# Performance work log

Measured on AMD Instinct MI355X. Metric: run time of the kernel, lower is better.

Reference implementation:

```python
import jax, jax.numpy as jnp
import numpy as np

B, LI, LC = 2, 1024, 256
H, NH, HD = 1024, 16, 64
MLP = 4096
EPS = 1e-6


def rmsnorm(x, w):
    return x * jax.lax.rsqrt(jnp.mean(x * x, axis=-1, keepdims=True) + EPS) * w


def apply_rope(x, cos, sin):
    # x: [B, NH, S, HD]; cos/sin: [S, HD]; rotate-half convention
    x1, x2 = jnp.split(x, 2, axis=-1)
    rot = jnp.concatenate([-x2, x1], axis=-1)
    return x * cos + rot * sin


def project_qkv(x, w, b):
    # x: [B, S, H] -> q,k,v each [B, NH, S, HD]
    bsz, s, _ = x.shape
    qkv = (x @ w.T + b).reshape(bsz, s, 3, NH, HD)
    qkv = jnp.transpose(qkv, (2, 0, 3, 1, 4))
    return qkv[0], qkv[1], qkv[2]


def setup_inputs() -> dict:
    key = jax.random.key(0)
    ks = iter(jax.random.split(key, 40))
    n = lambda shape, scale=1.0: jax.random.normal(next(ks), shape, dtype=jnp.float32) * scale
    xav = lambda fo, fi: n((fo, fi), float(np.sqrt(2.0 / (fo + fi))))
    inp = {
        'image_tokens': n((B, LI, H)),
        'condition_tokens': n((B, LC, H)),
        'image_rope_cos': n((LI, HD)),
        'image_rope_sin': n((LI, HD)),
        'cond_rope_cos': n((LC, HD)),
        'cond_rope_sin': n((LC, HD)),
        'img_norm1_w': jnp.ones((H,)), 'cond_norm1_w': jnp.ones((H,)),
        'img_qkv_w': xav(3 * H, H), 'img_qkv_b': jnp.zeros((3 * H,)),
        'cond_qkv_w': xav(3 * H, H), 'cond_qkv_b': jnp.zeros((3 * H,)),
        'img_qn_w': jnp.ones((HD,)), 'img_kn_w': jnp.ones((HD,)),
        'cond_qn_w': jnp.ones((HD,)), 'cond_kn_w': jnp.ones((HD,)),
        'img_out_w': xav(H, H), 'img_out_b': jnp.zeros((H,)),
        'cond_out_w': xav(H, H), 'cond_out_b': jnp.zeros((H,)),
        'img_norm2_w': jnp.ones((H,)), 'cond_norm2_w': jnp.ones((H,)),
        'img_mlp_w1': xav(MLP, H), 'img_mlp_b1': jnp.zeros((MLP,)),
        'img_mlp_w2': xav(MLP, H), 'img_mlp_b2': jnp.zeros((MLP,)),
        'img_mlp_w3': xav(H, MLP), 'img_mlp_b3': jnp.zeros((H,)),
        'cond_mlp_w1': xav(MLP, H), 'cond_mlp_b1': jnp.zeros((MLP,)),
        'cond_mlp_w2': xav(MLP, H), 'cond_mlp_b2': jnp.zeros((MLP,)),
        'cond_mlp_w3': xav(H, MLP), 'cond_mlp_b3': jnp.zeros((H,)),
        'alpha': jnp.zeros((1,)), 'beta': jnp.zeros((1,)),
    }
    return inp


def swiglu(x, w1, b1, w2, b2, w3, b3):
    return (jax.nn.silu(x @ w1.T + b1) * (x @ w2.T + b2)) @ w3.T + b3


def reference(image_tokens, condition_tokens, image_rope_cos, image_rope_sin,
              cond_rope_cos, cond_rope_sin, img_norm1_w, cond_norm1_w,
              img_qkv_w, img_qkv_b, cond_qkv_w, cond_qkv_b,
              img_qn_w, img_kn_w, cond_qn_w, cond_kn_w,
              img_out_w, img_out_b, cond_out_w, cond_out_b,
              img_norm2_w, cond_norm2_w,
              img_mlp_w1, img_mlp_b1, img_mlp_w2, img_mlp_b2, img_mlp_w3, img_mlp_b3,
              cond_mlp_w1, cond_mlp_b1, cond_mlp_w2, cond_mlp_b2, cond_mlp_w3, cond_mlp_b3,
              alpha, beta):
    img_res, cond_res = image_tokens, condition_tokens
    iq, ik, iv = project_qkv(rmsnorm(image_tokens, img_norm1_w), img_qkv_w, img_qkv_b)
    cq, ck, cv = project_qkv(rmsnorm(condition_tokens, cond_norm1_w), cond_qkv_w, cond_qkv_b)
    iq = apply_rope(rmsnorm(iq, img_qn_w), image_rope_cos, image_rope_sin)
    ik = apply_rope(rmsnorm(ik, img_kn_w), image_rope_cos, image_rope_sin)
    cq = apply_rope(rmsnorm(cq, cond_qn_w), cond_rope_cos, cond_rope_sin)
    ck = apply_rope(rmsnorm(ck, cond_kn_w), cond_rope_cos, cond_rope_sin)
    q = jnp.concatenate([cq, iq], axis=2)  # [B, NH, LC+LI, HD]
    k = jnp.concatenate([ck, ik], axis=2)
    v = jnp.concatenate([cv, iv], axis=2)
    scores = jnp.einsum('bhqd,bhkd->bhqk', q, k) / jnp.sqrt(jnp.float32(HD)).astype(q.dtype)
    attn = jax.nn.softmax(scores, axis=-1)
    out = jnp.einsum('bhqk,bhkd->bhqd', attn, v)
    cond_o, img_o = out[:, :, :LC], out[:, :, LC:]
    cond_o = jnp.transpose(cond_o, (0, 2, 1, 3)).reshape(B, LC, H)
    img_o = jnp.transpose(img_o, (0, 2, 1, 3)).reshape(B, LI, H)
    condition_tokens = cond_res + (cond_o @ cond_out_w.T + cond_out_b)
    image_tokens = img_res + alpha.reshape(1, 1, 1) * (img_o @ img_out_w.T + img_out_b)
    condition_tokens = condition_tokens + swiglu(rmsnorm(condition_tokens, cond_norm2_w),
                                                 cond_mlp_w1, cond_mlp_b1, cond_mlp_w2, cond_mlp_b2, cond_mlp_w3, cond_mlp_b3)
    image_tokens = image_tokens + beta.reshape(1, 1, 1) * swiglu(rmsnorm(image_tokens, img_norm2_w),
                                                                 img_mlp_w1, img_mlp_b1, img_mlp_w2, img_mlp_b2, img_mlp_w3, img_mlp_b3)
    return image_tokens, condition_tokens
```

## Files before the change

kernel.cpp:

```cpp
#include <hip/hip_runtime.h>
#include <hip/hip_bf16.h>

#define BB   2
#define LI   1024
#define LC   256
#define SEQ  1280
#define HDIM 1024
#define NH   16
#define HD   64
#define MLPD 4096
#define EPS  1e-6f
#define MROWS 2560
#define MTI  16
#define MTT  20

typedef __bf16 bf16x8 __attribute__((ext_vector_type(8)));
typedef float f32x4 __attribute__((ext_vector_type(4)));
typedef unsigned short us4 __attribute__((ext_vector_type(4)));
typedef unsigned short us8 __attribute__((ext_vector_type(8)));

static __device__ __forceinline__ unsigned short f2bf(float f) {
    unsigned int u = __builtin_bit_cast(unsigned int, f);
    u += 0x7fffu + ((u >> 16) & 1u);
    return (unsigned short)(u >> 16);
}
static __device__ __forceinline__ float bf2f(unsigned short h) {
    unsigned int u = ((unsigned int)h) << 16;
    return __builtin_bit_cast(float, u);
}

static __device__ __forceinline__ void gload_lds16(const void* g, void* l) {
    __builtin_amdgcn_global_load_lds((__attribute__((address_space(1))) void*)(g),
                                     (__attribute__((address_space(3))) void*)(l),
                                     16, 0, 0);
}

__global__ __launch_bounds__(256)
void pack_weights(const float* __restrict__ w1i, const float* __restrict__ w2i,
                  const float* __restrict__ w1c, const float* __restrict__ w2c,
                  const float* __restrict__ w3i, const float* __restrict__ w3c,
                  const float* __restrict__ wqi, const float* __restrict__ wqc,
                  const float* __restrict__ woi, const float* __restrict__ woc,
                  unsigned short* __restrict__ wpi, unsigned short* __restrict__ wpc,
                  unsigned short* __restrict__ w3bi, unsigned short* __restrict__ w3bc,
                  unsigned short* __restrict__ wqbi, unsigned short* __restrict__ wqbc,
                  unsigned short* __restrict__ wobi, unsigned short* __restrict__ wobc)
{
    const int seg = blockIdx.y;
    const float* s0 = nullptr; const float* s1 = nullptr;
    unsigned short* dst = nullptr; int n4 = 0; bool pair = false;
    switch (seg) {
        case 0: pair = true; s0 = w1i; s1 = w2i; dst = wpi;  n4 = 8388608 / 4; break;
        case 1: pair = true; s0 = w1c; s1 = w2c; dst = wpc;  n4 = 8388608 / 4; break;
        case 2: s0 = w3i; dst = w3bi; n4 = 4194304 / 4; break;
        case 3: s0 = w3c; dst = w3bc; n4 = 4194304 / 4; break;
        case 4: s0 = wqi; dst = wqbi; n4 = 3145728 / 4; break;
        case 5: s0 = wqc; dst = wqbc; n4 = 3145728 / 4; break;
        case 6: s0 = woi; dst = wobi; n4 = 1048576 / 4; break;
        case 7: s0 = woc; dst = wobc; n4 = 1048576 / 4; break;
    }
    for (int i = blockIdx.x * 256 + threadIdx.x; i < n4; i += gridDim.x * 256) {
        float4 v;
        if (pair) {
            int p  = i >> 8;
            int k4 = i & 255;
            int g = p >> 4, r = p & 15;
            const float* s = (g & 1) ? s1 : s0;
            v = *(const float4*)&s[((size_t)((g >> 1) * 16 + r)) * 1024 + k4 * 4];
        } else {
            v = ((const float4*)s0)[i];
        }
        us4 o = { f2bf(v.x), f2bf(v.y), f2bf(v.z), f2bf(v.w) };
        ((us4*)dst)[i] = o;
    }
}

__global__ __launch_bounds__(256)
void rmsnorm1(const float* __restrict__ img, const float* __restrict__ cond,
              const float* __restrict__ wi, const float* __restrict__ wc,
              unsigned short* __restrict__ xn)
{
    const int row = blockIdx.x;
    const int t   = threadIdx.x;
    const float* x = (row < 2048) ? img + (size_t)row * HDIM
                                  : cond + (size_t)(row - 2048) * HDIM;
    const float* w = (row < 2048) ? wi : wc;
    float4 v = ((const float4*)x)[t];
    float ss = v.x*v.x + v.y*v.y + v.z*v.z + v.w*v.w;
    for (int o = 32; o > 0; o >>= 1) ss += __shfl_xor(ss, o);
    __shared__ float red[4];
    if ((t & 63) == 0) red[t >> 6] = ss;
    __syncthreads();
    float inv = rsqrtf((red[0]+red[1]+red[2]+red[3]) * (1.0f / HDIM) + EPS);
    float4 wv = ((const float4*)w)[t];
    us4 pk = { f2bf(v.x*inv*wv.x), f2bf(v.y*inv*wv.y),
               f2bf(v.z*inv*wv.z), f2bf(v.w*inv*wv.w) };
    *(us4*)&xn[(size_t)row * HDIM + t * 4] = pk;
}

__global__ __launch_bounds__(256)
void rmsnorm2(const float* __restrict__ img_tok, const float* __restrict__ cond_tok,
              const float* __restrict__ op, const float* __restrict__ wi,
              const float* __restrict__ wc, const float* __restrict__ alpha,
              unsigned short* __restrict__ n2)
{
    const int row = blockIdx.x;
    const int t   = threadIdx.x;
    const bool img = row < 2048;
    const float sc = img ? alpha[0] : 1.0f;
    const float* tok = img ? img_tok + (size_t)row * HDIM
                           : cond_tok + (size_t)(row - 2048) * HDIM;
    const float* w = img ? wi : wc;
    float4 tv = ((const float4*)tok)[t];
    float4 ov = ((const float4*)(op + (size_t)row * HDIM))[t];
    float4 v = { tv.x + sc*ov.x, tv.y + sc*ov.y, tv.z + sc*ov.z, tv.w + sc*ov.w };
    float ss = v.x*v.x + v.y*v.y + v.z*v.z + v.w*v.w;
    for (int o = 32; o > 0; o >>= 1) ss += __shfl_xor(ss, o);
    __shared__ float red[4];
    if ((t & 63) == 0) red[t >> 6] = ss;
    __syncthreads();
    float inv = rsqrtf((red[0]+red[1]+red[2]+red[3]) * (1.0f / HDIM) + EPS);
    float4 wv = ((const float4*)w)[t];
    us4 pk = { f2bf(v.x*inv*wv.x), f2bf(v.y*inv*wv.y),
               f2bf(v.z*inv*wv.z), f2bf(v.w*inv*wv.w) };
    *(us4*)&n2[(size_t)row * HDIM + t * 4] = pk;
}

__global__ __launch_bounds__(256)
void op_init(const float* __restrict__ bi, const float* __restrict__ bc,
             float* __restrict__ op)
{
    const int row = blockIdx.x, t = threadIdx.x;
    const float* b = (row < 2048) ? bi : bc;
    ((float4*)(op + (size_t)row * HDIM))[t] = ((const float4*)b)[t];
}

__global__ __launch_bounds__(256)
void down_init(const float* __restrict__ img_tok, const float* __restrict__ cond_tok,
               const float* __restrict__ op, const float* __restrict__ b3i,
               const float* __restrict__ b3c, const float* __restrict__ alpha,
               const float* __restrict__ beta, float* __restrict__ out)
{
    const int row = blockIdx.x, t = threadIdx.x;
    const bool img = row < 2048;
    const float sa = img ? alpha[0] : 1.0f;
    const float sm = img ? beta[0]  : 1.0f;
    const float* tok = img ? img_tok + (size_t)row * HDIM
                           : cond_tok + (size_t)(row - 2048) * HDIM;
    const float* b3 = img ? b3i : b3c;
    float4 tv = ((const float4*)tok)[t];
    float4 ov = ((const float4*)(op + (size_t)row * HDIM))[t];
    float4 bv = ((const float4*)b3)[t];
    float4 o4 = { tv.x + sa*ov.x + sm*bv.x, tv.y + sa*ov.y + sm*bv.y,
                  tv.z + sa*ov.z + sm*bv.z, tv.w + sa*ov.w + sm*bv.w };
    ((float4*)(out + (size_t)row * HDIM))[t] = o4;
}

__global__ __launch_bounds__(256)
void qkv_gemm(const unsigned short* __restrict__ xn,
              const unsigned short* __restrict__ wqi, const unsigned short* __restrict__ wqc,
              const float* __restrict__ bi, const float* __restrict__ bc,
              unsigned short* __restrict__ qh, unsigned short* __restrict__ kh,
              unsigned short* __restrict__ vh)
{
    __shared__ __align__(16) unsigned short As[128][32];
    __shared__ __align__(16) unsigned short Ws[128][32];

    const int mt = blockIdx.x;
    const bool img = mt < MTI;
    const int row0 = img ? mt * 128 : 2048 + (mt - MTI) * 128;
    const int grow0 = img ? mt * 128 : (mt - MTI) * 128;
    const unsigned short* W = img ? wqi : wqc;
    const float* bias = img ? bi : bc;
    const int bn = blockIdx.y * 128;

    const int t = threadIdx.x, lane = t & 63, wid = t >> 6;
    const int wm = wid >> 1, wn = wid & 1;
    const int srow = (wid << 5) + (lane >> 2);
    const int scol = (lane & 3) << 3;
    const unsigned short* Ag0 = xn + (size_t)(row0 + srow)      * HDIM + scol;
    const unsigned short* Ag1 = xn + (size_t)(row0 + srow + 16) * HDIM + scol;
    const unsigned short* Wg0 = W  + (size_t)(bn + srow)        * HDIM + scol;
    const unsigned short* Wg1 = W  + (size_t)(bn + srow + 16)   * HDIM + scol;
    unsigned short* lA0 = &As[(wid << 5)     ][0];
    unsigned short* lA1 = &As[(wid << 5) + 16][0];
    unsigned short* lW0 = &Ws[(wid << 5)     ][0];
    unsigned short* lW1 = &Ws[(wid << 5) + 16][0];

    const int fr = lane & 15, kg = lane >> 4, ko = kg << 3;
    f32x4 acc[4][4] = {};

    for (int k0 = 0; k0 < HDIM; k0 += 32) {
        __syncthreads();
        gload_lds16(Ag0 + k0, lA0);
        gload_lds16(Ag1 + k0, lA1);
        gload_lds16(Wg0 + k0, lW0);
        gload_lds16(Wg1 + k0, lW1);
        __syncthreads();
        bf16x8 aF[4], bF[4];
#pragma unroll
        for (int m = 0; m < 4; ++m) aF[m] = *(const bf16x8*)&As[wm*64 + m*16 + fr][ko];
#pragma unroll
        for (int n = 0; n < 4; ++n) bF[n] = *(const bf16x8*)&Ws[wn*64 + n*16 + fr][ko];
#pragma unroll
        for (int m = 0; m < 4; ++m)
#pragma unroll
            for (int n = 0; n < 4; ++n)
                acc[m][n] = __builtin_amdgcn_mfma_f32_16x16x32_bf16(aF[m], bF[n], acc[m][n], 0,0,0);
    }

#pragma unroll
    for (int n = 0; n < 4; ++n) {
        const int gc = bn + wn*64 + n*16 + fr;
        const int which = gc >> 10;
        const int h = (gc >> 6) & 15, d = gc & 63;
        unsigned short* dst = which == 0 ? qh : (which == 1 ? kh : vh);
        const float bv = bias[gc];
#pragma unroll
        for (int m = 0; m < 4; ++m) {
#pragma unroll
            for (int j = 0; j < 4; ++j) {
                const int gl = grow0 + wm*64 + m*16 + (kg << 2) + j;
                int b, s;
                if (img) { b = gl >> 10; s = LC + (gl & 1023); }
                else     { b = gl >> 8;  s = gl & 255; }
                dst[(((size_t)(b*NH + h)) * SEQ + s) * HD + d] = f2bf(acc[m][n][j] + bv);
            }
        }
    }
}

__global__ __launch_bounds__(256)
void pair_gemm(const unsigned short* __restrict__ n2,
               const unsigned short* __restrict__ wpi, const unsigned short* __restrict__ wpc,
               const float* __restrict__ b1i, const float* __restrict__ b2i,
               const float* __restrict__ b1c, const float* __restrict__ b2c,
               unsigned short* __restrict__ hbf)
{
    __shared__ __align__(16) unsigned short As[128][32];
    __shared__ __align__(16) unsigned short Ws[128][32];

    const int mt = blockIdx.x;
    const bool img = mt < MTI;
    const int row0 = img ? mt * 128 : 2048 + (mt - MTI) * 128;
    const unsigned short* W = img ? wpi : wpc;
    const float* b1 = img ? b1i : b1c;
    const float* b2 = img ? b2i : b2c;
    const int x = blockIdx.y;
    const int bn = x * 128;

    const int t = threadIdx.x, lane = t & 63, wid = t >> 6;
    const int wm = wid >> 1, wn = wid & 1;
    const int srow = (wid << 5) + (lane >> 2);
    const int scol = (lane & 3) << 3;
    const unsigned short* Ag0 = n2 + (size_t)(row0 + srow)      * HDIM + scol;
    const unsigned short* Ag1 = n2 + (size_t)(row0 + srow + 16) * HDIM + scol;
    const unsigned short* Wg0 = W  + (size_t)(bn + srow)        * HDIM + scol;
    const unsigned short* Wg1 = W  + (size_t)(bn + srow + 16)   * HDIM + scol;
    unsigned short* lA0 = &As[(wid << 5)     ][0];
    unsigned short* lA1 = &As[(wid << 5) + 16][0];
    unsigned short* lW0 = &Ws[(wid << 5)     ][0];
    unsigned short* lW1 = &Ws[(wid << 5) + 16][0];

    const int fr = lane & 15, kg = lane >> 4, ko = kg << 3;
    f32x4 acc[4][4] = {};

    for (int k0 = 0; k0 < HDIM; k0 += 32) {
        __syncthreads();
        gload_lds16(Ag0 + k0, lA0);
        gload_lds16(Ag1 + k0, lA1);
        gload_lds16(Wg0 + k0, lW0);
        gload_lds16(Wg1 + k0, lW1);
        __syncthreads();
        bf16x8 aF[4], bF[4];
#pragma unroll
        for (int m = 0; m < 4; ++m) aF[m] = *(const bf16x8*)&As[wm*64 + m*16 + fr][ko];
#pragma unroll
        for (int n = 0; n < 4; ++n) bF[n] = *(const bf16x8*)&Ws[wn*64 + n*16 + fr][ko];
#pragma unroll
        for (int m = 0; m < 4; ++m)
#pragma unroll
            for (int n = 0; n < 4; ++n)
                acc[m][n] = __builtin_amdgcn_mfma_f32_16x16x32_bf16(aF[m], bF[n], acc[m][n], 0,0,0);
    }

#pragma unroll
    for (int p = 0; p < 2; ++p) {
        const int lc = (4*x + 2*wn + p) * 16 + fr;
        const float b1v = b1[lc], b2v = b2[lc];
#pragma unroll
        for (int m = 0; m < 4; ++m) {
#pragma unroll
            for (int j = 0; j < 4; ++j) {
                const int row = row0 + wm*64 + m*16 + (kg << 2) + j;
                float g1 = acc[m][2*p    ][j] + b1v;
                float g2 = acc[m][2*p + 1][j] + b2v;
                float hv = (g1 / (1.0f + __expf(-g1))) * g2;
                hbf[(size_t)row * MLPD + lc] = f2bf(hv);
            }
        }
    }
}

__global__ __launch_bounds__(256)
void nk_gemm(const unsigned short* __restrict__ A, int K,
             const unsigned short* __restrict__ Wimg, const unsigned short* __restrict__ Wcond,
             float* __restrict__ out, int kchunk,
             const float* __restrict__ sci, const float* __restrict__ scc)
{
    __shared__ __align__(16) unsigned short As[128][32];
    __shared__ __align__(16) unsigned short Ws[64][32];

    const int mt = blockIdx.x;
    const bool img = mt < MTI;
    const int row0 = img ? mt * 128 : 2048 + (mt - MTI) * 128;
    const unsigned short* W = img ? Wimg : Wcond;
    const float sc = img ? (sci ? sci[0] : 1.0f) : (scc ? scc[0] : 1.0f);
    const int bn = blockIdx.y * 64;
    const int kbase = blockIdx.z * kchunk;

    const int t = threadIdx.x, lane = t & 63, wid = t >> 6;
    const int srowA = (wid << 5) + (lane >> 2);
    const int srowW = (wid << 4) + (lane >> 2);
    const int scol  = (lane & 3) << 3;
    const unsigned short* Ag0 = A + (size_t)(row0 + srowA)      * K + kbase + scol;
    const unsigned short* Ag1 = A + (size_t)(row0 + srowA + 16) * K + kbase + scol;
    const unsigned short* Wg  = W + (size_t)(bn + srowW)        * K + kbase + scol;
    unsigned short* lA0 = &As[(wid << 5)     ][0];
    unsigned short* lA1 = &As[(wid << 5) + 16][0];
    unsigned short* lW  = &Ws[(wid << 4)     ][0];

    const int fr = lane & 15, kg = lane >> 4, ko = kg << 3;
    f32x4 acc[2][4] = {};

    for (int k0 = 0; k0 < kchunk; k0 += 32) {
        __syncthreads();
        gload_lds16(Ag0 + k0, lA0);
        gload_lds16(Ag1 + k0, lA1);
        gload_lds16(Wg  + k0, lW);
        __syncthreads();
        bf16x8 aF[2], bF[4];
#pragma unroll
        for (int m = 0; m < 2; ++m) aF[m] = *(const bf16x8*)&As[(wid<<5) + m*16 + fr][ko];
#pragma unroll
        for (int n = 0; n < 4; ++n) bF[n] = *(const bf16x8*)&Ws[n*16 + fr][ko];
#pragma unroll
        for (int m = 0; m < 2; ++m)
#pragma unroll
            for (int n = 0; n < 4; ++n)
                acc[m][n] = __builtin_amdgcn_mfma_f32_16x16x32_bf16(aF[m], bF[n], acc[m][n], 0,0,0);
    }

#pragma unroll
    for (int n = 0; n < 4; ++n) {
        const int col = bn + n*16 + fr;
#pragma unroll
        for (int m = 0; m < 2; ++m) {
#pragma unroll
            for (int j = 0; j < 4; ++j) {
                const int row = row0 + (wid << 5) + m*16 + (kg << 2) + j;
                unsafeAtomicAdd(&out[(size_t)row * HDIM + col], sc * acc[m][n][j]);
            }
        }
    }
}

__launch_bounds__(64)
__global__ void qkv_prep(unsigned short* __restrict__ qh, unsigned short* __restrict__ kh,
                         const float* __restrict__ img_qn, const float* __restrict__ img_kn,
                         const float* __restrict__ cond_qn, const float* __restrict__ cond_kn,
                         const float* __restrict__ icos, const float* __restrict__ isin,
                         const float* __restrict__ ccos, const float* __restrict__ csin)
{
    const int h = blockIdx.x, s = blockIdx.y, b = blockIdx.z;
    const int d = threadIdx.x;
    const float *qw, *kw, *cs, *sn;
    if (s < LC) { qw = cond_qn; kw = cond_kn;
                  cs = ccos + (size_t)s * HD; sn = csin + (size_t)s * HD; }
    else        { qw = img_qn; kw = img_kn;
                  cs = icos + (size_t)(s - LC) * HD; sn = isin + (size_t)(s - LC) * HD; }
    const size_t idx = (((size_t)(b*NH + h)) * SEQ + s) * HD + d;
    float qv = bf2f(qh[idx]);
    float kv = bf2f(kh[idx]);

    float sq = qv * qv;
    for (int o = 32; o > 0; o >>= 1) sq += __shfl_xor(sq, o);
    float qn = qv * rsqrtf(sq * (1.0f / HD) + EPS) * qw[d];
    float sk = kv * kv;
    for (int o = 32; o > 0; o >>= 1) sk += __shfl_xor(sk, o);
    float kn = kv * rsqrtf(sk * (1.0f / HD) + EPS) * kw[d];

    const float c = cs[d], s_ = sn[d];
    float qp = __shfl_xor(qn, 32);
    float kp = __shfl_xor(kn, 32);
    float qrot = (d < 32) ? -qp : qp;
    float krot = (d < 32) ? -kp : kp;
    qh[idx] = f2bf((qn * c + qrot * s_) * 0.125f);
    kh[idx] = f2bf(kn * c + krot * s_);
}

__global__ __launch_bounds__(256)
void transpose_v(const unsigned short* __restrict__ vb, unsigned short* __restrict__ vt)
{
    const int bh = blockIdx.y;
    const int s0 = blockIdx.x * 64;
    const int t  = threadIdx.x;
    __shared__ unsigned short tile[64][72];
#pragma unroll
    for (int i = 0; i < 2; ++i) {
        int e = t + i * 256;
        int r = e >> 3, c8 = (e & 7) * 8;
        us8 v = *(const us8*)&vb[((size_t)bh * SEQ + s0 + r) * HD + c8];
        *(us8*)&tile[r][c8] = v;
    }
    __syncthreads();
#pragma unroll
    for (int i = 0; i < 2; ++i) {
        int e = t + i * 256;
        int d = e >> 3, c8 = (e & 7) * 8;
        us8 pk;
#pragma unroll
        for (int j = 0; j < 8; ++j) pk[j] = tile[c8 + j][d];
        *(us8*)&vt[((size_t)bh * HD + d) * SEQ + s0 + c8] = pk;
    }
}

__global__ __launch_bounds__(128)
void attn_mfma(const unsigned short* __restrict__ qg,
               const unsigned short* __restrict__ kg,
               const unsigned short* __restrict__ vtg,
               unsigned short* __restrict__ o)
{
    const int q0  = blockIdx.x * 64;
    const int h   = blockIdx.y;
    const int b   = blockIdx.z;
    const int bh  = b * NH + h;
    const int t   = threadIdx.x;
    const int wid = t >> 6;
    const int lane = t & 63;
    const int g  = lane >> 4;
    const int fr = lane & 15;

    __shared__ __align__(16) unsigned short Ks [64 * 64];
    __shared__ __align__(16) unsigned short VTs[64 * 64];
    __shared__ __align__(16) unsigned short Ps [2][32][72];

    const unsigned short* qb  = qg  + (size_t)bh * SEQ * HD;
    const unsigned short* kb  = kg  + (size_t)bh * SEQ * HD;
    const unsigned short* vtb = vtg + (size_t)bh * HD * SEQ;

    bf16x8 Qf[2][2];
#pragma unroll
    for (int mt = 0; mt < 2; ++mt)
#pragma unroll
        for (int kc = 0; kc < 2; ++kc)
            Qf[mt][kc] = *(const bf16x8*)&qb[(size_t)(q0 + wid*32 + mt*16 + fr) * HD
                                             + kc*32 + g*8];

    f32x4 O[2][4] = {};
    float mrow[2][4], lrow[2][4];
#pragma unroll
    for (int mt = 0; mt < 2; ++mt)
#pragma unroll
        for (int rg = 0; rg < 4; ++rg) { mrow[mt][rg] = -3e38f; lrow[mt][rg] = 0.f; }

    for (int tile = 0; tile < SEQ / 64; ++tile) {
        __syncthreads();
#pragma unroll
        for (int i = 0; i < 4; ++i) {
            int ch = t + i * 128;
            int r = ch >> 3, c = ch & 7;
            int cs = c ^ (r & 7);
            gload_lds16(kb  + (size_t)(tile*64 + r) * HD + cs*8,
                        Ks  + ((i*128 + wid*64) << 3));
            gload_lds16(vtb + (size_t)r * SEQ + tile*64 + cs*8,
                        VTs + ((i*128 + wid*64) << 3));
        }
        __syncthreads();

        f32x4 S[2][4] = {};
#pragma unroll
        for (int kc = 0; kc < 2; ++kc)
#pragma unroll
            for (int nt = 0; nt < 4; ++nt) {
                int r = fr + 16*nt;
                bf16x8 kf = *(const bf16x8*)&Ks[r*64 + (((g + 4*kc) ^ (r & 7)) * 8)];
#pragma unroll
                for (int mt = 0; mt < 2; ++mt)
                    S[mt][nt] = __builtin_amdgcn_mfma_f32_16x16x32_bf16(
                        Qf[mt][kc], kf, S[mt][nt], 0, 0, 0);
            }

#pragma unroll
        for (int mt = 0; mt < 2; ++mt) {
            float al[4];
#pragma unroll
            for (int rg = 0; rg < 4; ++rg) {
                float tm = fmaxf(fmaxf(S[mt][0][rg], S[mt][1][rg]),
                                 fmaxf(S[mt][2][rg], S[mt][3][rg]));
#pragma unroll
                for (int off = 1; off < 16; off <<= 1) tm = fmaxf(tm, __shfl_xor(tm, off));
                float mn = fmaxf(mrow[mt][rg], tm);
                al[rg] = __expf(mrow[mt][rg] - mn);
                mrow[mt][rg] = mn;
            }
#pragma unroll
            for (int rg = 0; rg < 4; ++rg) {
#pragma unroll
                for (int nt = 0; nt < 4; ++nt)
                    S[mt][nt][rg] = __expf(S[mt][nt][rg] - mrow[mt][rg]);
                float s0 = S[mt][0][rg] + S[mt][1][rg] + S[mt][2][rg] + S[mt][3][rg];
#pragma unroll
                for (int off = 1; off < 16; off <<= 1) s0 += __shfl_xor(s0, off);
                lrow[mt][rg] = al[rg] * lrow[mt][rg] + s0;
            }
#pragma unroll
            for (int dt = 0; dt < 4; ++dt)
#pragma unroll
                for (int rg = 0; rg < 4; ++rg) O[mt][dt][rg] *= al[rg];
#pragma unroll
            for (int nt = 0; nt < 4; ++nt)
#pragma unroll
                for (int rg = 0; rg < 4; ++rg)
                    Ps[wid][mt*16 + 4*g + rg][16*nt + fr] = f2bf(S[mt][nt][rg]);
        }

#pragma unroll
        for (int kc = 0; kc < 2; ++kc) {
            bf16x8 Pf[2];
#pragma unroll
            for (int mt = 0; mt < 2; ++mt)
                Pf[mt] = *(const bf16x8*)&Ps[wid][mt*16 + fr][kc*32 + g*8];
#pragma unroll
            for (int dt = 0; dt < 4; ++dt) {
                int r = fr + 16*dt;
                bf16x8 vf = *(const bf16x8*)&VTs[r*64 + (((g + 4*kc) ^ (r & 7)) * 8)];
#pragma unroll
                for (int mt = 0; mt < 2; ++mt)
                    O[mt][dt] = __builtin_amdgcn_mfma_f32_16x16x32_bf16(
                        Pf[mt], vf, O[mt][dt], 0, 0, 0);
            }
        }
    }

#pragma unroll
    for (int mt = 0; mt < 2; ++mt)
#pragma unroll
        for (int rg = 0; rg < 4; ++rg) {
            const int s_tok = q0 + wid*32 + mt*16 + 4*g + rg;
            const float linv = 1.0f / lrow[mt][rg];
            const size_t row = (s_tok < LC) ? (size_t)(2048 + b*LC + s_tok)
                                            : (size_t)(b*LI + (s_tok - LC));
#pragma unroll
            for (int dt = 0; dt < 4; ++dt)
                o[row * HDIM + h*HD + 16*dt + fr] = f2bf(O[mt][dt][rg] * linv);
        }
}

extern "C" void kernel_launch(void* const* d_in, const int* in_sizes, int n_in,
                              void* d_out, int out_size, void* d_ws, size_t ws_size,
                              hipStream_t stream)
{
    const float* image_tokens = (const float*)d_in[0];
    const float* cond_tokens  = (const float*)d_in[1];
    const float* icos  = (const float*)d_in[2];
    const float* isin  = (const float*)d_in[3];
    const float* ccos  = (const float*)d_in[4];
    const float* csin  = (const float*)d_in[5];
    const float* img_n1w  = (const float*)d_in[6];
    const float* cond_n1w = (const float*)d_in[7];
    const float* img_qkv_w  = (const float*)d_in[8];
    const float* img_qkv_b  = (const float*)d_in[9];
    const float* cond_qkv_w = (const float*)d_in[10];
    const float* cond_qkv_b = (const float*)d_in[11];
    const float* img_qn  = (const float*)d_in[12];
    const float* img_kn  = (const float*)d_in[13];
    const float* cond_qn = (const float*)d_in[14];
    const float* cond_kn = (const float*)d_in[15];
    const float* img_out_w  = (const float*)d_in[16];
    const float* img_out_b  = (const float*)d_in[17];
    const float* cond_out_w = (const float*)d_in[18];
    const float* cond_out_b = (const float*)d_in[19];
    const float* img_n2w  = (const float*)d_in[20];
    const float* cond_n2w = (const float*)d_in[21];
    const float* img_w1 = (const float*)d_in[22];
    const float* img_b1 = (const float*)d_in[23];
    const float* img_w2 = (const float*)d_in[24];
    const float* img_b2 = (const float*)d_in[25];
    const float* img_w3 = (const float*)d_in[26];
    const float* img_b3 = (const float*)d_in[27];
    const float* cond_w1 = (const float*)d_in[28];
    const float* cond_b1 = (const float*)d_in[29];
    const float* cond_w2 = (const float*)d_in[30];
    const float* cond_b2 = (const float*)d_in[31];
    const float* cond_w3 = (const float*)d_in[32];
    const float* cond_b3 = (const float*)d_in[33];
    const float* alpha = (const float*)d_in[34];
    const float* beta  = (const float*)d_in[35];

    float* out = (float*)d_out;

    unsigned short* u = (unsigned short*)d_ws;
    unsigned short* wp_i  = u + 0;
    unsigned short* wp_c  = u + 8388608;
    unsigned short* w3b_i = u + 16777216;
    unsigned short* w3b_c = u + 20971520;
    unsigned short* wqb_i = u + 25165824;
    unsigned short* wqb_c = u + 28311552;
    unsigned short* wob_i = u + 31457280;
    unsigned short* wob_c = u + 32505856;
    const size_t A0 = 33554432;
    unsigned short* xn = u + A0;
    unsigned short* vt = u + A0;
    unsigned short* qh = u + A0 + 2621440;
    unsigned short* kh = u + A0 + 5242880;
    unsigned short* vh = u + A0 + 7864320;
    unsigned short* o  = u + A0 + 10485760;
    float*          op = (float*)(u + A0 + 2621440);
    unsigned short* n2 = u + A0 + 7864320;
    unsigned short* hbf = u + 25165824;

    pack_weights<<<dim3(512, 8), 256, 0, stream>>>(
        img_w1, img_w2, cond_w1, cond_w2, img_w3, cond_w3,
        img_qkv_w, cond_qkv_w, img_out_w, cond_out_w,
        wp_i, wp_c, w3b_i, w3b_c, wqb_i, wqb_c, wob_i, wob_c);

    rmsnorm1<<<MROWS, 256, 0, stream>>>(image_tokens, cond_tokens, img_n1w, cond_n1w, xn);

    qkv_gemm<<<dim3(MTT, 24), 256, 0, stream>>>(
        xn, wqb_i, wqb_c, img_qkv_b, cond_qkv_b, qh, kh, vh);

    qkv_prep<<<dim3(NH, SEQ, BB), 64, 0, stream>>>(
        qh, kh, img_qn, img_kn, cond_qn, cond_kn, icos, isin, ccos, csin);
    transpose_v<<<dim3(SEQ / 64, BB * NH), 256, 0, stream>>>(vh, vt);

    attn_mfma<<<dim3(SEQ / 64, NH, BB), 128, 0, stream>>>(qh, kh, vt, o);

    op_init<<<MROWS, 256, 0, stream>>>(img_out_b, cond_out_b, op);
    nk_gemm<<<dim3(MTT, 16, 2), 256, 0, stream>>>(
        o, HDIM, wob_i, wob_c, op, HDIM / 2, nullptr, nullptr);

    rmsnorm2<<<MROWS, 256, 0, stream>>>(
        image_tokens, cond_tokens, op, img_n2w, cond_n2w, alpha, n2);

    pair_gemm<<<dim3(MTT, 64), 256, 0, stream>>>(
        n2, wp_i, wp_c, img_b1, img_b2, cond_b1, cond_b2, hbf);

    down_init<<<MROWS, 256, 0, stream>>>(
        image_tokens, cond_tokens, op, img_b3, cond_b3, alpha, beta, out);
    nk_gemm<<<dim3(MTT, 16, 4), 256, 0, stream>>>(
        hbf, MLPD, w3b_i, w3b_c, out, MLPD / 4, beta, nullptr);
}
```

Before: 321.7 us.

## Fuse V transpose into QKV GEMM and double-buffer attention K/V tiles

The QKV GEMM epilogue now writes V straight into the transposed [d][seq] layout, which removes the separate transpose_v kernel and its extra pass over memory. The attention kernel uses 256-thread blocks covering 128 queries, double-buffers the K/V tiles in LDS so the next tile loads during compute, and computes S transposed so row max and sum reduce within a thread. qkv_prep packs four heads-rows per block to cut launch and block overhead. The workspace buffers are laid out again so vt no longer aliases xn. Risks include lower occupancy from the larger LDS footprint and fewer attention blocks (320).

```diff
diff --git a/kernel.cpp b/kernel.cpp
--- a/kernel.cpp
+++ b/kernel.cpp
@@ -161,7 +161,7 @@
               const unsigned short* __restrict__ wqi, const unsigned short* __restrict__ wqc,
               const float* __restrict__ bi, const float* __restrict__ bc,
               unsigned short* __restrict__ qh, unsigned short* __restrict__ kh,
-              unsigned short* __restrict__ vh)
+              unsigned short* __restrict__ vt)
 {
     __shared__ __align__(16) unsigned short As[128][32];
     __shared__ __align__(16) unsigned short Ws[128][32];
@@ -214,17 +214,22 @@
         const int gc = bn + wn*64 + n*16 + fr;
         const int which = gc >> 10;
         const int h = (gc >> 6) & 15, d = gc & 63;
-        unsigned short* dst = which == 0 ? qh : (which == 1 ? kh : vh);
         const float bv = bias[gc];
 #pragma unroll
         for (int m = 0; m < 4; ++m) {
-#pragma unroll
-            for (int j = 0; j < 4; ++j) {
-                const int gl = grow0 + wm*64 + m*16 + (kg << 2) + j;
-                int b, s;
-                if (img) { b = gl >> 10; s = LC + (gl & 1023); }
-                else     { b = gl >> 8;  s = gl & 255; }
-                dst[(((size_t)(b*NH + h)) * SEQ + s) * HD + d] = f2bf(acc[m][n][j] + bv);
+            const int gl0 = grow0 + wm*64 + m*16 + (kg << 2);
+            int b, s0;
+            if (img) { b = gl0 >> 10; s0 = LC + (gl0 & 1023); }
+            else     { b = gl0 >> 8;  s0 = gl0 & 255; }
+            if (which == 2) {
+                us4 pk = { f2bf(acc[m][n][0] + bv), f2bf(acc[m][n][1] + bv),
+                           f2bf(acc[m][n][2] + bv), f2bf(acc[m][n][3] + bv) };
+                *(us4*)&vt[(((size_t)(b*NH + h)) * HD + d) * SEQ + s0] = pk;
+            } else {
+                unsigned short* dst = (which == 0) ? qh : kh;
+#pragma unroll
+                for (int j = 0; j < 4; ++j)
+                    dst[(((size_t)(b*NH + h)) * SEQ + s0 + j) * HD + d] = f2bf(acc[m][n][j] + bv);
             }
         }
     }
@@ -365,15 +370,20 @@
     }
 }
 
-__launch_bounds__(64)
+__launch_bounds__(256)
 __global__ void qkv_prep(unsigned short* __restrict__ qh, unsigned short* __restrict__ kh,
                          const float* __restrict__ img_qn, const float* __restrict__ img_kn,
                          const float* __restrict__ cond_qn, const float* __restrict__ cond_kn,
                          const float* __restrict__ icos, const float* __restrict__ isin,
                          const float* __restrict__ ccos, const float* __restrict__ csin)
 {
-    const int h = blockIdx.x, s = blockIdx.y, b = blockIdx.z;
-    const int d = threadIdx.x;
+    const int L = blockIdx.x * 4 + (threadIdx.x >> 6);
+    const int d = threadIdx.x & 63;
+    const int b = L / (NH * SEQ);
+    const int rem = L - b * NH * SEQ;
+    const int h = rem / SEQ;
+    const int s = rem - h * SEQ;
+
     const float *qw, *kw, *cs, *sn;
     if (s < LC) { qw = cond_qn; kw = cond_kn;
                   cs = ccos + (size_t)s * HD; sn = csin + (size_t)s * HD; }
@@ -400,38 +410,12 @@
 }
 
 __global__ __launch_bounds__(256)
-void transpose_v(const unsigned short* __restrict__ vb, unsigned short* __restrict__ vt)
-{
-    const int bh = blockIdx.y;
-    const int s0 = blockIdx.x * 64;
-    const int t  = threadIdx.x;
-    __shared__ unsigned short tile[64][72];
-#pragma unroll
-    for (int i = 0; i < 2; ++i) {
-        int e = t + i * 256;
-        int r = e >> 3, c8 = (e & 7) * 8;
-        us8 v = *(const us8*)&vb[((size_t)bh * SEQ + s0 + r) * HD + c8];
-        *(us8*)&tile[r][c8] = v;
-    }
-    __syncthreads();
-#pragma unroll
-    for (int i = 0; i < 2; ++i) {
-        int e = t + i * 256;
-        int d = e >> 3, c8 = (e & 7) * 8;
-        us8 pk;
-#pragma unroll
-        for (int j = 0; j < 8; ++j) pk[j] = tile[c8 + j][d];
-        *(us8*)&vt[((size_t)bh * HD + d) * SEQ + s0 + c8] = pk;
-    }
-}
-
-__global__ __launch_bounds__(128)
 void attn_mfma(const unsigned short* __restrict__ qg,
                const unsigned short* __restrict__ kg,
                const unsigned short* __restrict__ vtg,
                unsigned short* __restrict__ o)
 {
-    const int q0  = blockIdx.x * 64;
+    const int q0  = blockIdx.x * 128;
     const int h   = blockIdx.y;
     const int b   = blockIdx.z;
     const int bh  = b * NH + h;
@@ -441,9 +425,9 @@
     const int g  = lane >> 4;
     const int fr = lane & 15;
 
-    __shared__ __align__(16) unsigned short Ks [64 * 64];
-    __shared__ __align__(16) unsigned short VTs[64 * 64];
-    __shared__ __align__(16) unsigned short Ps [2][32][72];
+    __shared__ __align__(16) unsigned short Ks [2][64 * 64];
+    __shared__ __align__(16) unsigned short VTs[2][64 * 64];
+    __shared__ __align__(16) unsigned short Ps [4][32][72];
 
     const unsigned short* qb  = qg  + (size_t)bh * SEQ * HD;
     const unsigned short* kb  = kg  + (size_t)bh * SEQ * HD;
@@ -458,71 +442,80 @@
                                              + kc*32 + g*8];
 
     f32x4 O[2][4] = {};
-    float mrow[2][4], lrow[2][4];
-#pragma unroll
-    for (int mt = 0; mt < 2; ++mt)
-#pragma unroll
-        for (int rg = 0; rg < 4; ++rg) { mrow[mt][rg] = -3e38f; lrow[mt][rg] = 0.f; }
+    float mreg[2] = { -3e38f, -3e38f };
+    float lreg[2] = { 0.f, 0.f };
+
+#define STAGE(tile_, bufi_)                                                     \
+    {                                                                           \
+        _Pragma("unroll")                                                       \
+        for (int i = 0; i < 2; ++i) {                                           \
+            int chbase = i * 256 + wid * 64;                                    \
+            int ch = chbase + lane;                                             \
+            int r = ch >> 3, c = ch & 7;                                        \
+            int cs_ = c ^ (r & 7);                                              \
+            gload_lds16(kb  + (size_t)((tile_)*64 + r) * HD + cs_*8,            \
+                        &Ks[bufi_][chbase * 8]);                                \
+            gload_lds16(vtb + (size_t)r * SEQ + (tile_)*64 + cs_*8,             \
+                        &VTs[bufi_][chbase * 8]);                               \
+        }                                                                       \
+    }
+
+    STAGE(0, 0);
+    __syncthreads();
+    int buf = 0;
 
     for (int tile = 0; tile < SEQ / 64; ++tile) {
-        __syncthreads();
-#pragma unroll
-        for (int i = 0; i < 4; ++i) {
-            int ch = t + i * 128;
-            int r = ch >> 3, c = ch & 7;
-            int cs = c ^ (r & 7);
-            gload_lds16(kb  + (size_t)(tile*64 + r) * HD + cs*8,
-                        Ks  + ((i*128 + wid*64) << 3));
-            gload_lds16(vtb + (size_t)r * SEQ + tile*64 + cs*8,
-                        VTs + ((i*128 + wid*64) << 3));
-        }
-        __syncthreads();
-
-        f32x4 S[2][4] = {};
+        if (tile + 1 < SEQ / 64) STAGE(tile + 1, buf ^ 1);
+
+        f32x4 ST[2][4] = {};
 #pragma unroll
         for (int kc = 0; kc < 2; ++kc)
 #pragma unroll
             for (int nt = 0; nt < 4; ++nt) {
                 int r = fr + 16*nt;
-                bf16x8 kf = *(const bf16x8*)&Ks[r*64 + (((g + 4*kc) ^ (r & 7)) * 8)];
+                bf16x8 kf = *(const bf16x8*)&Ks[buf][r*64 + (((g + 4*kc) ^ (r & 7)) * 8)];
 #pragma unroll
                 for (int mt = 0; mt < 2; ++mt)
-                    S[mt][nt] = __builtin_amdgcn_mfma_f32_16x16x32_bf16(
-                        Qf[mt][kc], kf, S[mt][nt], 0, 0, 0);
+                    ST[mt][nt] = __builtin_amdgcn_mfma_f32_16x16x32_bf16(
+                        kf, Qf[mt][kc], ST[mt][nt], 0, 0, 0);
             }
 
 #pragma unroll
         for (int mt = 0; mt < 2; ++mt) {
-            float al[4];
-#pragma unroll
-            for (int rg = 0; rg < 4; ++rg) {
-                float tm = fmaxf(fmaxf(S[mt][0][rg], S[mt][1][rg]),
-                                 fmaxf(S[mt][2][rg], S[mt][3][rg]));
-#pragma unroll
-                for (int off = 1; off < 16; off <<= 1) tm = fmaxf(tm, __shfl_xor(tm, off));
-                float mn = fmaxf(mrow[mt][rg], tm);
-                al[rg] = __expf(mrow[mt][rg] - mn);
-                mrow[mt][rg] = mn;
+            float tm = -3e38f;
+#pragma unroll
+            for (int nt = 0; nt < 4; ++nt)
+#pragma unroll
+                for (int j = 0; j < 4; ++j) tm = fmaxf(tm, ST[mt][nt][j]);
+            tm = fmaxf(tm, __shfl_xor(tm, 16));
+            tm = fmaxf(tm, __shfl_xor(tm, 32));
+            float mn = fmaxf(mreg[mt], tm);
+            float al = __expf(mreg[mt] - mn);
+            mreg[mt] = mn;
+            float ls = 0.f;
+#pragma unroll
+            for (int nt = 0; nt < 4; ++nt) {
+#pragma unroll
+                for (int j = 0; j < 4; ++j) {
+                    float p = __expf(ST[mt][nt][j] - mn);
+                    ST[mt][nt][j] = p;
+                    ls += p;
+                }
             }
-#pragma unroll
-            for (int rg = 0; rg < 4; ++rg) {
-#pragma unroll
-                for (int nt = 0; nt < 4; ++nt)
-                    S[mt][nt][rg] = __expf(S[mt][nt][rg] - mrow[mt][rg]);
-                float s0 = S[mt][0][rg] + S[mt][1][rg] + S[mt][2][rg] + S[mt][3][rg];
-#pragma unroll
-                for (int off = 1; off < 16; off <<= 1) s0 += __shfl_xor(s0, off);
-                lrow[mt][rg] = al[rg] * lrow[mt][rg] + s0;
+            ls += __shfl_xor(ls, 16);
+            ls += __shfl_xor(ls, 32);
+            lreg[mt] = al * lreg[mt] + ls;
+            f32x4 alr;
+#pragma unroll
+            for (int rg = 0; rg < 4; ++rg) alr[rg] = __shfl(al, 4*g + rg);
+#pragma unroll
+            for (int dt = 0; dt < 4; ++dt) O[mt][dt] *= alr;
+#pragma unroll
+            for (int nt = 0; nt < 4; ++nt) {
+                us4 pk = { f2bf(ST[mt][nt][0]), f2bf(ST[mt][nt][1]),
+                           f2bf(ST[mt][nt][2]), f2bf(ST[mt][nt][3]) };
+                *(us4*)&Ps[wid][mt*16 + fr][16*nt + 4*g] = pk;
             }
-#pragma unroll
-            for (int dt = 0; dt < 4; ++dt)
-#pragma unroll
-                for (int rg = 0; rg < 4; ++rg) O[mt][dt][rg] *= al[rg];
-#pragma unroll
-            for (int nt = 0; nt < 4; ++nt)
-#pragma unroll
-                for (int rg = 0; rg < 4; ++rg)
-                    Ps[wid][mt*16 + 4*g + rg][16*nt + fr] = f2bf(S[mt][nt][rg]);
         }
 
 #pragma unroll
@@ -534,27 +527,35 @@
 #pragma unroll
             for (int dt = 0; dt < 4; ++dt) {
                 int r = fr + 16*dt;
-                bf16x8 vf = *(const bf16x8*)&VTs[r*64 + (((g + 4*kc) ^ (r & 7)) * 8)];
+                bf16x8 vf = *(const bf16x8*)&VTs[buf][r*64 + (((g + 4*kc) ^ (r & 7)) * 8)];
 #pragma unroll
                 for (int mt = 0; mt < 2; ++mt)
                     O[mt][dt] = __builtin_amdgcn_mfma_f32_16x16x32_bf16(
                         Pf[mt], vf, O[mt][dt], 0, 0, 0);
             }
         }
-    }
-
-#pragma unroll
-    for (int mt = 0; mt < 2; ++mt)
+
+        __syncthreads();
+        buf ^= 1;
+    }
+
+#pragma unroll
+    for (int mt = 0; mt < 2; ++mt) {
+        const float linv = 1.0f / lreg[mt];
+        f32x4 lv;
+#pragma unroll
+        for (int rg = 0; rg < 4; ++rg) lv[rg] = __shfl(linv, 4*g + rg);
 #pragma unroll
         for (int rg = 0; rg < 4; ++rg) {
             const int s_tok = q0 + wid*32 + mt*16 + 4*g + rg;
-            const float linv = 1.0f / lrow[mt][rg];
             const size_t row = (s_tok < LC) ? (size_t)(2048 + b*LC + s_tok)
                                             : (size_t)(b*LI + (s_tok - LC));
 #pragma unroll
             for (int dt = 0; dt < 4; ++dt)
-                o[row * HDIM + h*HD + 16*dt + fr] = f2bf(O[mt][dt][rg] * linv);
+                o[row * HDIM + h*HD + 16*dt + fr] = f2bf(O[mt][dt][rg] * lv[rg]);
         }
+    }
+#undef STAGE
 }
 
 extern "C" void kernel_launch(void* const* d_in, const int* in_sizes, int n_in,
@@ -609,15 +610,13 @@
     unsigned short* wqb_c = u + 28311552;
     unsigned short* wob_i = u + 31457280;
     unsigned short* wob_c = u + 32505856;
-    const size_t A0 = 33554432;
-    unsigned short* xn = u + A0;
-    unsigned short* vt = u + A0;
-    unsigned short* qh = u + A0 + 2621440;
-    unsigned short* kh = u + A0 + 5242880;
-    unsigned short* vh = u + A0 + 7864320;
-    unsigned short* o  = u + A0 + 10485760;
-    float*          op = (float*)(u + A0 + 2621440);
-    unsigned short* n2 = u + A0 + 7864320;
+    unsigned short* xn = u + 33554432;
+    unsigned short* vt = u + 36175872;
+    unsigned short* qh = u + 38797312;
+    unsigned short* kh = u + 41418752;
+    unsigned short* o  = u + 44040192;
+    float*          op = (float*)(u + 38797312);
+    unsigned short* n2 = u + 36175872;
     unsigned short* hbf = u + 25165824;
 
     pack_weights<<<dim3(512, 8), 256, 0, stream>>>(
@@ -628,13 +627,12 @@
     rmsnorm1<<<MROWS, 256, 0, stream>>>(image_tokens, cond_tokens, img_n1w, cond_n1w, xn);
 
     qkv_gemm<<<dim3(MTT, 24), 256, 0, stream>>>(
-        xn, wqb_i, wqb_c, img_qkv_b, cond_qkv_b, qh, kh, vh);
-
-    qkv_prep<<<dim3(NH, SEQ, BB), 64, 0, stream>>>(
+        xn, wqb_i, wqb_c, img_qkv_b, cond_qkv_b, qh, kh, vt);
+
+    qkv_prep<<<BB * NH * SEQ / 4, 256, 0, stream>>>(
         qh, kh, img_qn, img_kn, cond_qn, cond_kn, icos, isin, ccos, csin);
-    transpose_v<<<dim3(SEQ / 64, BB * NH), 256, 0, stream>>>(vh, vt);
-
-    attn_mfma<<<dim3(SEQ / 64, NH, BB), 128, 0, stream>>>(qh, kh, vt, o);
+
+    attn_mfma<<<dim3(SEQ / 128, NH, BB), 256, 0, stream>>>(qh, kh, vt, o);
 
     op_init<<<MROWS, 256, 0, stream>>>(img_out_b, cond_out_b, op);
     nk_gemm<<<dim3(MTT, 16, 2), 256, 0, stream>>>(
```

Measured after the change: 294.5 us. 8.4% less time.
